# Optimization experiments

Hardware: AMD Instinct MI355X
Metric: run time of the kernel (lower is better)

The kernel has to match this reference:

```python
import jax, jax.numpy as jnp
import numpy as np

N_COMPANY, N_INDUSTRY, E = 20000, 500, 8192
CC, CI, D, H = 256, 128, 256, 4


def setup_inputs() -> dict:
    key = jax.random.key(0)
    ks = jax.random.split(key, 14)
    p = lambda k, shape: (jax.random.normal(k, shape, jnp.float32) * 0.02)
    company_x = jax.random.normal(ks[0], (N_COMPANY, CC), jnp.float32)
    industry_x = jax.random.normal(ks[1], (N_INDUSTRY, CI), jnp.float32)
    src = jax.random.randint(ks[2], (E,), 0, N_COMPANY)
    tgt = jax.random.randint(ks[3], (E,), 0, N_INDUSTRY)
    edge_index = jnp.stack([src, tgt]).astype(jnp.int64)
    return {
        "company_x": company_x,
        "industry_x": industry_x,
        "edge_index": edge_index,
        "Wc": p(ks[4], (D, CC)), "bc": jnp.zeros((D,), jnp.float32),
        "Wi": p(ks[5], (D, CI)), "bi": jnp.zeros((D,), jnp.float32),
        "w_in": p(ks[6], (3 * D, D)), "b_in": jnp.zeros((3 * D,), jnp.float32),
        "w_out": p(ks[7], (D, D)), "b_out": jnp.zeros((D,), jnp.float32),
        "gamma": jnp.ones((D,), jnp.float32), "beta": jnp.zeros((D,), jnp.float32),
    }


def reference(company_x, industry_x, edge_index, Wc, bc, Wi, bi, w_in, b_in, w_out, b_out, gamma, beta):
    company_h = company_x @ Wc.T + bc          # [N, D]
    industry_h = industry_x @ Wi.T + bi        # [M, D]
    src, tgt = edge_index[0], edge_index[1]
    e = src.shape[0]
    d = company_h.shape[-1]
    hd = d // H

    q_in = company_h[src]                      # [E, D] gather
    kv_in = industry_h[tgt]                    # [E, D] gather

    wq, wk, wv = jnp.split(w_in, 3, axis=0)
    bq, bk, bv = jnp.split(b_in, 3)
    qh = (q_in @ wq.T + bq).reshape(e, H, hd)
    kh = (kv_in @ wk.T + bk).reshape(e, H, hd)
    vh = (kv_in @ wv.T + bv).reshape(e, H, hd)

    scale = 1.0 / jnp.sqrt(jnp.float32(hd))
    scores = jnp.einsum("qhd,khd->hqk", qh * scale, kh)   # [H, E, E]
    attn = jax.nn.softmax(scores, axis=-1)
    ctx = jnp.einsum("hqk,khd->qhd", attn, vh).reshape(e, d)
    attn_out = ctx @ w_out.T + b_out                        # [E, D]

    agg = jax.ops.segment_sum(attn_out, src, num_segments=company_h.shape[0])
    counts = jax.ops.segment_sum(jnp.ones((e,), jnp.float32), src, num_segments=company_h.shape[0])
    pooled = agg / (counts[:, None] + 1e-6)

    out = company_h + pooled
    mean = out.mean(-1, keepdims=True)
    var = out.var(-1, keepdims=True)
    return (out - mean) / jnp.sqrt(var + 1e-5) * gamma + beta
```

## Files before the change

### kernel.cpp

```cpp
#include <hip/hip_runtime.h>

#define E_EDGES 8192
#define N_COMP  20000
#define N_IND   500
#define NKEYS   512

typedef short bf16x8 __attribute__((ext_vector_type(8)));
typedef float f32x4  __attribute__((ext_vector_type(4)));

static __device__ __forceinline__ unsigned short f2bf(float v) {
    unsigned u = __builtin_bit_cast(unsigned, v);
    u = (u + 0x7FFFu + ((u >> 16) & 1u)) >> 16;
    return (unsigned short)u;
}

static __device__ __forceinline__ void cvt8(const float* __restrict__ s,
                                            unsigned short* __restrict__ d) {
    float4 a = *(const float4*)s;
    float4 b = *(const float4*)(s + 4);
    bf16x8 o;
    o[0] = (short)f2bf(a.x); o[1] = (short)f2bf(a.y);
    o[2] = (short)f2bf(a.z); o[3] = (short)f2bf(a.w);
    o[4] = (short)f2bf(b.x); o[5] = (short)f2bf(b.y);
    o[6] = (short)f2bf(b.z); o[7] = (short)f2bf(b.w);
    *(bf16x8*)d = o;
}

static __device__ __forceinline__ bf16x8 cvt8r(const float* __restrict__ s) {
    float4 a = *(const float4*)s;
    float4 b = *(const float4*)(s + 4);
    bf16x8 v;
    v[0] = (short)f2bf(a.x); v[1] = (short)f2bf(a.y);
    v[2] = (short)f2bf(a.z); v[3] = (short)f2bf(a.w);
    v[4] = (short)f2bf(b.x); v[5] = (short)f2bf(b.y);
    v[6] = (short)f2bf(b.z); v[7] = (short)f2bf(b.w);
    return v;
}

#define SWZ(r)   (((r) & 7) << 4)
#define SWZ4(r)  ((((r) >> 1) & 3) << 4)

static __device__ __forceinline__ void stage_f32(const float* src, char* base,
                                                 int sr, int sc) {
    *(bf16x8*)(base + ((sr * 64 + sc * 2) ^ SWZ(sr))) = cvt8r(src);
}

__global__ __launch_bounds__(256) void prep(
    const int* __restrict__ src, const int* __restrict__ tgt,
    const float* __restrict__ Wc, const float* __restrict__ Wi,
    const float* __restrict__ w_out, const float* __restrict__ w_in,
    const float* __restrict__ bc, const float* __restrict__ bi,
    const float* __restrict__ b_in,
    float* __restrict__ csrc, float* __restrict__ ctgt,
    unsigned short* __restrict__ Wc_bf, unsigned short* __restrict__ wout_bf,
    unsigned short* __restrict__ WcT_bf, unsigned short* __restrict__ Wi_bf,
    unsigned short* __restrict__ wkv_bf, float* __restrict__ beff)
{
    const int bid = blockIdx.x, tid = threadIdx.x;
    if (bid < 32) {
        int e = bid * 256 + tid;
        atomicAdd(&csrc[src[e]], 1.0f);
        atomicAdd(&ctgt[tgt[e]], 1.0f);
    } else if (bid < 64) {
        long i = ((long)(bid - 32) * 256 + tid) * 8;
        cvt8(Wc + i, Wc_bf + i);
    } else if (bid < 96) {
        long i = ((long)(bid - 64) * 256 + tid) * 8;
        cvt8(w_out + i, wout_bf + i);
    } else if (bid < 128) {
        long o = ((long)(bid - 96) * 256 + tid) * 8;
        int c = (int)(o >> 8), d0 = (int)(o & 255);
        bf16x8 v;
#pragma unroll
        for (int j = 0; j < 8; j++) v[j] = (short)f2bf(Wc[(long)(d0 + j) * 256 + c]);
        *(bf16x8*)(WcT_bf + o) = v;
    } else if (bid < 144) {
        long i = ((long)(bid - 128) * 256 + tid) * 8;
        cvt8(Wi + i, Wi_bf + i);
    } else if (bid < 208) {
        long i = ((long)(bid - 144) * 256 + tid) * 8;
        cvt8(w_in + 65536 + i, wkv_bf + i);
    } else {
        int gi = (bid - 208) * 256 + tid;
        int e = gi >> 2, q = gi & 3;
        const float* base = (e < 256) ? bc : bi;
        const float* wr = w_in + (long)e * 256 + q * 64;
        const float* br = base + q * 64;
        float s = 0.f;
#pragma unroll
        for (int j = 0; j < 64; j += 4) {
            float4 w4 = *(const float4*)(wr + j);
            float4 b4 = *(const float4*)(br + j);
            s += w4.x * b4.x + w4.y * b4.y + w4.z * b4.z + w4.w * b4.w;
        }
        s += __shfl_xor(s, 1);
        s += __shfl_xor(s, 2);
        if (q == 0) beff[e] = s + b_in[e];
    }
}

__global__ __launch_bounds__(256) void fusedW(
    const float* __restrict__ w_in, const unsigned short* __restrict__ WcT_bf,
    const float* __restrict__ industry_x, const unsigned short* __restrict__ Wi_bf,
    const unsigned short* __restrict__ wkv_bf, const float* __restrict__ beff,
    const float* __restrict__ ctgt, const float* __restrict__ csrc,
    unsigned short* __restrict__ Wcq_bf, unsigned short* __restrict__ Kbuf,
    unsigned short* __restrict__ VTg,
    float* __restrict__ cntT, int* __restrict__ list, int* __restrict__ nlist)
{
    const int bid = blockIdx.x;
    if (bid >= 20) {
        int i = (bid - 20) * 256 + threadIdx.x;
        if (i < NKEYS) cntT[(i & 15) * 32 + (i >> 4)] = ctgt[i];
        if (i < N_COMP && csrc[i] > 0.f) {
            int k = atomicAdd(nlist, 1);
            list[k] = i;
        }
        return;
    }

    __shared__ char lds[48 * 1024];
    const int t = threadIdx.x, wv = t >> 6, lane = t & 63;
    const int g = lane >> 4, ln = lane & 15;
    const int sr = t >> 2, sc = (t & 3) * 8;

    if (bid < 4) {
        char* ab = lds;
        char* wb = lds + 4 * 1024;
        const int bm = bid * 64;
        f32x4 acc[16];
#pragma unroll
        for (int i = 0; i < 16; i++) acc[i] = (f32x4){0.f, 0.f, 0.f, 0.f};
        const float* aptr = w_in + (long)(bm + sr) * 256 + sc;
        for (int kc = 0; kc < 256; kc += 32) {
            __syncthreads();
            stage_f32(aptr + kc, ab, sr, sc);
#pragma unroll
            for (int p = 0; p < 4; p++) {
                int r = p * 64 + sr;
                *(bf16x8*)(wb + ((r * 64 + sc * 2) ^ SWZ(r))) =
                    *(const bf16x8*)(WcT_bf + (long)r * 256 + kc + sc);
            }
            __syncthreads();
            int ar = wv * 16 + ln;
            bf16x8 af = *(bf16x8*)(ab + ((ar * 64 + g * 16) ^ SWZ(ar)));
#pragma unroll
            for (int nj = 0; nj < 16; nj++) {
                int wr = nj * 16 + ln;
                bf16x8 bf = *(bf16x8*)(wb + ((wr * 64 + g * 16) ^ SWZ(wr)));
                acc[nj] = __builtin_amdgcn_mfma_f32_16x16x32_bf16(af, bf, acc[nj], 0, 0, 0);
            }
        }
#pragma unroll
        for (int nj = 0; nj < 16; nj++)
#pragma unroll
            for (int r = 0; r < 4; r++)
                Wcq_bf[(long)(bm + wv * 16 + g * 4 + r) * 256 + nj * 16 + ln] =
                    f2bf(acc[nj][r]);
        return;
    }

    const int rg = (bid - 4) >> 1, colh = (bid - 4) & 1;
    char* ab  = lds;
    char* wb1 = lds + 4 * 1024;
    char* ihb = lds + 16 * 1024;
    char* wb2 = lds;

    {
        f32x4 a1[16];
#pragma unroll
        for (int i = 0; i < 16; i++) a1[i] = (f32x4){0.f, 0.f, 0.f, 0.f};
        int arow = rg * 64 + sr; if (arow > N_IND - 1) arow = N_IND - 1;
        const float* aptr = industry_x + (long)arow * 128 + sc;
        for (int kc = 0; kc < 128; kc += 32) {
            __syncthreads();
            stage_f32(aptr + kc, ab, sr, sc);
#pragma unroll
            for (int p = 0; p < 4; p++) {
                int r = p * 64 + sr;
                *(bf16x8*)(wb1 + ((r * 64 + sc * 2) ^ SWZ(r))) =
                    *(const bf16x8*)(Wi_bf + (long)r * 128 + kc + sc);
            }
            __syncthreads();
            int ar = wv * 16 + ln;
            bf16x8 af = *(bf16x8*)(ab + ((ar * 64 + g * 16) ^ SWZ(ar)));
#pragma unroll
            for (int nj = 0; nj < 16; nj++) {
                int wr = nj * 16 + ln;
                bf16x8 bf = *(bf16x8*)(wb1 + ((wr * 64 + g * 16) ^ SWZ(wr)));
                a1[nj] = __builtin_amdgcn_mfma_f32_16x16x32_bf16(af, bf, a1[nj], 0, 0, 0);
            }
        }
        __syncthreads();
#pragma unroll
        for (int nj = 0; nj < 16; nj++)
#pragma unroll
            for (int r = 0; r < 4; r++) {
                int row = wv * 16 + g * 4 + r, col = nj * 16 + ln;
                *(unsigned short*)(ihb + ((row * 512 + col * 2) ^ SWZ(row))) =
                    f2bf(a1[nj][r]);
            }
    }
    __syncthreads();

    if (colh == 0) {
        f32x4 a2[16];
#pragma unroll
        for (int i = 0; i < 16; i++) a2[i] = (f32x4){0.f, 0.f, 0.f, 0.f};
        for (int kc = 0; kc < 256; kc += 32) {
            __syncthreads();
#pragma unroll
            for (int p = 0; p < 4; p++) {
                int r = p * 64 + sr;
                *(bf16x8*)(wb2 + ((r * 64 + sc * 2) ^ SWZ(r))) =
                    *(const bf16x8*)(wkv_bf + (long)r * 256 + kc + sc);
            }
            __syncthreads();
            int row = wv * 16 + ln;
            bf16x8 af = *(bf16x8*)(ihb + ((row * 512 + (kc + g * 8) * 2) ^ SWZ(row)));
#pragma unroll
            for (int nj = 0; nj < 16; nj++) {
                int wr = nj * 16 + ln;
                bf16x8 bf = *(bf16x8*)(wb2 + ((wr * 64 + g * 16) ^ SWZ(wr)));
                a2[nj] = __builtin_amdgcn_mfma_f32_16x16x32_bf16(af, bf, a2[nj], 0, 0, 0);
            }
        }
#pragma unroll
        for (int nj = 0; nj < 16; nj++)
#pragma unroll
            for (int r = 0; r < 4; r++) {
                int R = rg * 64 + wv * 16 + g * 4 + r, n = nj * 16 + ln;
                Kbuf[(long)R * 256 + n] = f2bf(a2[nj][r] + beff[256 + n]);
            }
    } else {
        const unsigned short* wp = wkv_bf + 65536;
        f32x4 a2[16];
#pragma unroll
        for (int i = 0; i < 16; i++) a2[i] = (f32x4){0.f, 0.f, 0.f, 0.f};
        for (int kc = 0; kc < 256; kc += 32) {
            __syncthreads();
#pragma unroll
            for (int p = 0; p < 4; p++) {
                int r = p * 64 + sr;
                *(bf16x8*)(wb2 + ((r * 64 + sc * 2) ^ SWZ(r))) =
                    *(const bf16x8*)(wp + (long)r * 256 + kc + sc);
            }
            __syncthreads();
#pragma unroll
            for (int mi = 0; mi < 4; mi++) {
                int arow = wv * 64 + mi * 16 + ln;
                bf16x8 af = *(bf16x8*)(wb2 + ((arow * 64 + g * 16) ^ SWZ(arow)));
#pragma unroll
                for (int t4 = 0; t4 < 4; t4++) {
                    int brow = t4 * 16 + ln;
                    bf16x8 bfr = *(bf16x8*)(ihb + ((brow * 512 + (kc + g * 8) * 2) ^ SWZ(brow)));
                    a2[mi * 4 + t4] = __builtin_amdgcn_mfma_f32_16x16x32_bf16(af, bfr, a2[mi * 4 + t4], 0, 0, 0);
                }
            }
        }
#pragma unroll
        for (int mi = 0; mi < 4; mi++)
#pragma unroll
            for (int t4 = 0; t4 < 4; t4++)
#pragma unroll
                for (int r = 0; r < 4; r++) {
                    int nrow = wv * 64 + mi * 16 + g * 4 + r;
                    VTg[(long)nrow * 512 + rg * 64 + t4 * 16 + ln] =
                        f2bf(a2[mi * 4 + t4][r] + beff[512 + nrow]);
                }
    }
}

__global__ __launch_bounds__(256, 2) void megattn(
    const float* __restrict__ company_x,
    const unsigned short* __restrict__ Wcq,
    const float* __restrict__ beff,
    const unsigned short* __restrict__ Kbuf,
    const unsigned short* __restrict__ VTg,
    const float* __restrict__ cntT,
    const unsigned short* __restrict__ wout,
    const float* __restrict__ b_out,
    const int* __restrict__ list, const int* __restrict__ nlist,
    float* __restrict__ pooled)
{
    const int M = *nlist;
    const int bm = blockIdx.x * 16;
    if (bm >= M) return;

    __shared__ char lds[24576];
    const int t = threadIdx.x, h = t >> 6, lane = t & 63;
    const int g = lane >> 4, ln = lane & 15;
    char* qbase = lds + h * 2048;
    char* xbase = lds + 8192;
    char* pbase = lds + 16384 + h * 2048;

    {
        int row = t >> 4, c0 = (t & 15) * 16;
        int mr = bm + row; if (mr > M - 1) mr = M - 1;
        const float* src = company_x + (long)list[mr] * 256 + c0;
        *(bf16x8*)(xbase + ((row * 512 + c0 * 2) ^ SWZ(row))) = cvt8r(src);
        *(bf16x8*)(xbase + ((row * 512 + c0 * 2 + 16) ^ SWZ(row))) = cvt8r(src + 8);
    }
    __syncthreads();

    bf16x8 qf0, qf1;
    {
        f32x4 qa[4];
#pragma unroll
        for (int i = 0; i < 4; i++) qa[i] = (f32x4){0.f, 0.f, 0.f, 0.f};
#pragma unroll
        for (int kc = 0; kc < 256; kc += 32) {
            bf16x8 af = *(bf16x8*)(xbase + ((ln * 512 + (kc + g * 8) * 2) ^ SWZ(ln)));
#pragma unroll
            for (int nj = 0; nj < 4; nj++) {
                bf16x8 bf = *(const bf16x8*)(Wcq + (long)(h * 64 + nj * 16 + ln) * 256 + kc + g * 8);
                qa[nj] = __builtin_amdgcn_mfma_f32_16x16x32_bf16(af, bf, qa[nj], 0, 0, 0);
            }
        }
#pragma unroll
        for (int nj = 0; nj < 4; nj++)
#pragma unroll
            for (int r = 0; r < 4; r++) {
                int row = g * 4 + r, col = nj * 16 + ln;
                *(unsigned short*)(qbase + ((row * 128 + col * 2) ^ SWZ(row))) =
                    f2bf((qa[nj][r] + beff[h * 64 + col]) * 0.125f);
            }
        qf0 = *(bf16x8*)(qbase + ((ln * 128 + g * 16) ^ SWZ(ln)));
        qf1 = *(bf16x8*)(qbase + ((ln * 128 + 64 + g * 16) ^ SWZ(ln)));
    }

    f32x4 acc[4];
#pragma unroll
    for (int i = 0; i < 4; i++) acc[i] = (f32x4){0.f, 0.f, 0.f, 0.f};
    float mreg[4] = {-1e30f, -1e30f, -1e30f, -1e30f};
    float lreg[4] = {0.f, 0.f, 0.f, 0.f};

#pragma unroll
    for (int tile = 0; tile < 2; tile++) {
        f32x4 S[8][2];
#pragma unroll
        for (int c = 0; c < 8; c++)
#pragma unroll
            for (int sub = 0; sub < 2; sub++) {
                const unsigned short* kr =
                    Kbuf + (long)(tile * 256 + c * 32 + sub * 16 + ln) * 256 + h * 64 + g * 8;
                bf16x8 k0 = *(const bf16x8*)(kr);
                bf16x8 k1 = *(const bf16x8*)(kr + 32);
                f32x4 s = (f32x4){0.f, 0.f, 0.f, 0.f};
                s = __builtin_amdgcn_mfma_f32_16x16x32_bf16(qf0, k0, s, 0, 0, 0);
                s = __builtin_amdgcn_mfma_f32_16x16x32_bf16(qf1, k1, s, 0, 0, 0);
                S[c][sub] = s;
            }

        float cnt[16];
        {
            const float* cp = cntT + ln * 32 + tile * 16;
#pragma unroll
            for (int j4 = 0; j4 < 4; j4++) {
                float4 c4 = *(const float4*)(cp + j4 * 4);
                cnt[j4 * 4 + 0] = c4.x; cnt[j4 * 4 + 1] = c4.y;
                cnt[j4 * 4 + 2] = c4.z; cnt[j4 * 4 + 3] = c4.w;
            }
        }

        float tm[4] = {-1e30f, -1e30f, -1e30f, -1e30f};
#pragma unroll
        for (int c = 0; c < 8; c++)
#pragma unroll
            for (int sub = 0; sub < 2; sub++)
#pragma unroll
                for (int r = 0; r < 4; r++) tm[r] = fmaxf(tm[r], S[c][sub][r]);
#pragma unroll
        for (int st = 1; st < 16; st <<= 1)
#pragma unroll
            for (int r = 0; r < 4; r++) tm[r] = fmaxf(tm[r], __shfl_xor(tm[r], st));

        float corr[4];
#pragma unroll
        for (int r = 0; r < 4; r++) {
            float mn = fmaxf(mreg[r], tm[r]);
            corr[r] = __expf(mreg[r] - mn);
            mreg[r] = mn;
        }

        float ps[4] = {0.f, 0.f, 0.f, 0.f};
#pragma unroll
        for (int c = 0; c < 8; c++)
#pragma unroll
            for (int sub = 0; sub < 2; sub++) {
                float cv = cnt[c * 2 + sub];
#pragma unroll
                for (int r = 0; r < 4; r++) {
                    float p = cv * __expf(S[c][sub][r] - mreg[r]);
                    S[c][sub][r] = p;
                    ps[r] += p;
                }
            }
#pragma unroll
        for (int st = 1; st < 16; st <<= 1)
#pragma unroll
            for (int r = 0; r < 4; r++) ps[r] += __shfl_xor(ps[r], st);
#pragma unroll
        for (int r = 0; r < 4; r++) lreg[r] = lreg[r] * corr[r] + ps[r];
#pragma unroll
        for (int i = 0; i < 4; i++)
#pragma unroll
            for (int r = 0; r < 4; r++) acc[i][r] *= corr[r];

#pragma unroll
        for (int c = 0; c < 8; c++) {
            char* pb = pbase + (c & 1) * 1024;
#pragma unroll
            for (int sub = 0; sub < 2; sub++)
#pragma unroll
                for (int r = 0; r < 4; r++) {
                    int row = g * 4 + r;
                    *(unsigned short*)(pb + ((row * 64 + (sub * 16 + ln) * 2) ^ SWZ4(row))) =
                        f2bf(S[c][sub][r]);
                }
            bf16x8 pa = *(bf16x8*)(pb + ((ln * 64 + g * 16) ^ SWZ4(ln)));
#pragma unroll
            for (int t4 = 0; t4 < 4; t4++) {
                bf16x8 vf = *(const bf16x8*)(
                    VTg + (long)(h * 64 + t4 * 16 + ln) * 512 + tile * 256 + c * 32 + g * 8);
                acc[t4] = __builtin_amdgcn_mfma_f32_16x16x32_bf16(pa, vf, acc[t4], 0, 0, 0);
            }
        }
    }

#pragma unroll
    for (int t4 = 0; t4 < 4; t4++)
#pragma unroll
        for (int r = 0; r < 4; r++) {
            int row = g * 4 + r, col = t4 * 16 + ln;
            *(unsigned short*)(qbase + ((row * 128 + col * 2) ^ SWZ(row))) =
                f2bf(acc[t4][r] / lreg[r]);
        }
    __syncthreads();

    {
        f32x4 oa[4];
#pragma unroll
        for (int i = 0; i < 4; i++) oa[i] = (f32x4){0.f, 0.f, 0.f, 0.f};
#pragma unroll
        for (int kc = 0; kc < 256; kc += 32) {
            int hs = kc >> 6;
            int off = (kc & 63) + g * 8;
            bf16x8 af = *(bf16x8*)(lds + hs * 2048 + ((ln * 128 + off * 2) ^ SWZ(ln)));
#pragma unroll
            for (int nj = 0; nj < 4; nj++) {
                bf16x8 bf = *(const bf16x8*)(wout + (long)(h * 64 + nj * 16 + ln) * 256 + kc + g * 8);
                oa[nj] = __builtin_amdgcn_mfma_f32_16x16x32_bf16(af, bf, oa[nj], 0, 0, 0);
            }
        }
#pragma unroll
        for (int nj = 0; nj < 4; nj++) {
            int n = h * 64 + nj * 16 + ln;
            float bv = b_out[n];
#pragma unroll
            for (int r = 0; r < 4; r++) {
                int R = bm + g * 4 + r;
                if (R < M)
                    pooled[(long)list[R] * 256 + n] = oa[nj][r] + bv;
            }
        }
    }
}

__global__ __launch_bounds__(256) void gemm_ln(
    const float* __restrict__ A, const unsigned short* __restrict__ W,
    const float* __restrict__ bias,
    const float* __restrict__ pooled, const float* __restrict__ csrc,
    const float* __restrict__ gamma, const float* __restrict__ beta,
    float* __restrict__ out, int M, int K)
{
    __shared__ unsigned short As[64 * 32];
    __shared__ unsigned short Ws[256 * 32];
    char* abase = (char*)As;
    char* wbase = (char*)Ws;

    const int bm = blockIdx.x * 64;
    const int t = threadIdx.x;
    const int wv = t >> 6, lane = t & 63, g = lane >> 4, ln = lane & 15;

    f32x4 acc[16];
#pragma unroll
    for (int i = 0; i < 16; i++) acc[i] = (f32x4){0.f, 0.f, 0.f, 0.f};

    const int sr = t >> 2;
    const int sc = (t & 3) * 8;
    int arow = bm + sr; if (arow > M - 1) arow = M - 1;
    const float* aptr = A + (long)arow * K + sc;

    for (int kc = 0; kc < K; kc += 32) {
        __syncthreads();
        stage_f32(aptr + kc, abase, sr, sc);
#pragma unroll
        for (int p = 0; p < 4; p++) {
            int r = p * 64 + sr;
            *(bf16x8*)(wbase + ((r * 64 + sc * 2) ^ SWZ(r))) =
                *(const bf16x8*)(W + (long)r * K + kc + sc);
        }
        __syncthreads();

        const int ar = wv * 16 + ln;
        bf16x8 af = *(bf16x8*)(abase + ((ar * 64 + g * 16) ^ SWZ(ar)));
#pragma unroll
        for (int nj = 0; nj < 16; nj++) {
            int wr = nj * 16 + ln;
            bf16x8 bf = *(bf16x8*)(wbase + ((wr * 64 + g * 16) ^ SWZ(wr)));
            acc[nj] = __builtin_amdgcn_mfma_f32_16x16x32_bf16(af, bf, acc[nj], 0, 0, 0);
        }
    }

#pragma unroll
    for (int r = 0; r < 4; r++) {
        int R = bm + wv * 16 + g * 4 + r;
        bool valid = R < M;
        int Rc = valid ? R : 0;
        float cntv = csrc[Rc];
        float factor = (valid && cntv > 0.f) ? cntv / (cntv + 1e-6f) : 0.f;

        float v[16];
        float sum = 0.f, sq = 0.f;
#pragma unroll
        for (int nj = 0; nj < 16; nj++) {
            int n = nj * 16 + ln;
            float x = acc[nj][r] + bias[n] + factor * pooled[(long)Rc * 256 + n];
            v[nj] = x;
            sum += x;
            sq  += x * x;
        }
#pragma unroll
        for (int st = 1; st < 16; st <<= 1) {
            sum += __shfl_xor(sum, st);
            sq  += __shfl_xor(sq,  st);
        }
        float mean = sum * (1.0f / 256.0f);
        float var  = sq * (1.0f / 256.0f) - mean * mean;
        float rstd = rsqrtf(var + 1e-5f);
        if (valid) {
#pragma unroll
            for (int nj = 0; nj < 16; nj++) {
                int n = nj * 16 + ln;
                out[(long)R * 256 + n] = (v[nj] - mean) * rstd * gamma[n] + beta[n];
            }
        }
    }
}

extern "C" void kernel_launch(void* const* d_in, const int* in_sizes, int n_in,
                              void* d_out, int out_size, void* d_ws, size_t ws_size,
                              hipStream_t stream)
{
    const float* company_x  = (const float*)d_in[0];
    const float* industry_x = (const float*)d_in[1];
    const int*   edge       = (const int*)d_in[2];
    const float* Wc         = (const float*)d_in[3];
    const float* bc         = (const float*)d_in[4];
    const float* Wi         = (const float*)d_in[5];
    const float* bi         = (const float*)d_in[6];
    const float* w_in       = (const float*)d_in[7];
    const float* b_in       = (const float*)d_in[8];
    const float* w_out      = (const float*)d_in[9];
    const float* b_out      = (const float*)d_in[10];
    const float* gamma      = (const float*)d_in[11];
    const float* beta       = (const float*)d_in[12];
    float* out = (float*)d_out;

    const int* src = edge;
    const int* tgt = edge + E_EDGES;

    float* wf = (float*)d_ws;
    size_t o = 0;
    unsigned short* Wc_bf   = (unsigned short*)(wf + o); o += 32768;
    unsigned short* wout_bf = (unsigned short*)(wf + o); o += 32768;
    unsigned short* WcT_bf  = (unsigned short*)(wf + o); o += 32768;
    unsigned short* Wi_bf   = (unsigned short*)(wf + o); o += 16384;
    unsigned short* wkv_bf  = (unsigned short*)(wf + o); o += 65536;
    unsigned short* Wcq_bf  = (unsigned short*)(wf + o); o += 32768;
    unsigned short* Kbuf    = (unsigned short*)(wf + o); o += 65536;
    unsigned short* VTg     = (unsigned short*)(wf + o); o += 65536;
    float* pooled           = wf + o; o += (size_t)N_COMP * 256;
    float* beff             = wf + o; o += 768;
    float* cntT             = wf + o; o += NKEYS;
    int*   list             = (int*)(wf + o); o += E_EDGES;
    float* csrc             = wf + o; o += N_COMP;
    float* ctgt             = wf + o; o += NKEYS;
    int*   nlist            = (int*)(wf + o); o += 4;

    dim3 blk(256);

    hipMemsetAsync(csrc, 0, (N_COMP + NKEYS + 4) * sizeof(float), stream);

    prep<<<dim3(220), blk, 0, stream>>>(
        src, tgt, Wc, Wi, w_out, w_in, bc, bi, b_in,
        csrc, ctgt, Wc_bf, wout_bf, WcT_bf, Wi_bf, wkv_bf, beff);

    fusedW<<<dim3(99), blk, 0, stream>>>(
        w_in, WcT_bf, industry_x, Wi_bf, wkv_bf, beff, ctgt, csrc,
        Wcq_bf, Kbuf, VTg, cntT, list, nlist);

    megattn<<<dim3(E_EDGES / 16), blk, 0, stream>>>(
        company_x, Wcq_bf, beff, Kbuf, VTg, cntT, wout_bf, b_out,
        list, nlist, pooled);

    gemm_ln<<<dim3((N_COMP + 63) / 64), blk, 0, stream>>>(
        company_x, Wc_bf, bc, pooled, csrc, gamma, beta, out, N_COMP, 256);
}
```

Measured before the change: 103.5 us.

## Split attention key range across two wave groups with split-K softmax merge

The megattn block grows from 256 to 512 threads. Each head now gets two waves, and each wave handles one half of the 512 keys instead of looping over both tiles. Partial max, sum and context accumulators from the second half go through LDS and are merged with log-sum-exp rescaling. The output projection is then split across all 8 waves. This doubles the waves per block to hide latency, at the cost of more LDS (56KB), an extra barrier and the merge step, which may limit occupancy.

```diff
diff --git a/kernel.cpp b/kernel.cpp
--- a/kernel.cpp
+++ b/kernel.cpp
@@ -271,7 +271,7 @@
     }
 }
 
-__global__ __launch_bounds__(256, 2) void megattn(
+__global__ __launch_bounds__(512, 4) void megattn(
     const float* __restrict__ company_x,
     const unsigned short* __restrict__ Wcq,
     const float* __restrict__ beff,
@@ -287,19 +287,24 @@
     const int bm = blockIdx.x * 16;
     if (bm >= M) return;
 
-    __shared__ char lds[24576];
-    const int t = threadIdx.x, h = t >> 6, lane = t & 63;
-    const int g = lane >> 4, ln = lane & 15;
+    __shared__ char lds[57344];
+    const int t = threadIdx.x;
+    const int w = t >> 6;
+    const int h = w & 3;
+    const int ks = w >> 2;
+    const int lane = t & 63, g = lane >> 4, ln = lane & 15;
+
     char* qbase = lds + h * 2048;
     char* xbase = lds + 8192;
-    char* pbase = lds + 16384 + h * 2048;
+    char* pbase = lds + 16384 + w * 2048;
+    float* macc = (float*)(lds + 32768) + h * 1024;
+    float* mml  = (float*)(lds + 49152) + h * 512;
 
     {
-        int row = t >> 4, c0 = (t & 15) * 16;
+        int row = t >> 5, c0 = (t & 31) * 8;
         int mr = bm + row; if (mr > M - 1) mr = M - 1;
         const float* src = company_x + (long)list[mr] * 256 + c0;
         *(bf16x8*)(xbase + ((row * 512 + c0 * 2) ^ SWZ(row))) = cvt8r(src);
-        *(bf16x8*)(xbase + ((row * 512 + c0 * 2 + 16) ^ SWZ(row))) = cvt8r(src + 8);
     }
     __syncthreads();
 
@@ -322,140 +327,149 @@
 #pragma unroll
             for (int r = 0; r < 4; r++) {
                 int row = g * 4 + r, col = nj * 16 + ln;
+                *(unsigned short*)(pbase + ((row * 128 + col * 2) ^ SWZ(row))) =
+                    f2bf((qa[nj][r] + beff[h * 64 + col]) * 0.125f);
+            }
+        qf0 = *(bf16x8*)(pbase + ((ln * 128 + g * 16) ^ SWZ(ln)));
+        qf1 = *(bf16x8*)(pbase + ((ln * 128 + 64 + g * 16) ^ SWZ(ln)));
+    }
+
+    f32x4 S[8][2];
+#pragma unroll
+    for (int c = 0; c < 8; c++)
+#pragma unroll
+        for (int sub = 0; sub < 2; sub++) {
+            const unsigned short* kr =
+                Kbuf + (long)(ks * 256 + c * 32 + sub * 16 + ln) * 256 + h * 64 + g * 8;
+            bf16x8 k0 = *(const bf16x8*)(kr);
+            bf16x8 k1 = *(const bf16x8*)(kr + 32);
+            f32x4 s = (f32x4){0.f, 0.f, 0.f, 0.f};
+            s = __builtin_amdgcn_mfma_f32_16x16x32_bf16(qf0, k0, s, 0, 0, 0);
+            s = __builtin_amdgcn_mfma_f32_16x16x32_bf16(qf1, k1, s, 0, 0, 0);
+            S[c][sub] = s;
+        }
+
+    float cnt[16];
+    {
+        const float* cp = cntT + ln * 32 + ks * 16;
+#pragma unroll
+        for (int j4 = 0; j4 < 4; j4++) {
+            float4 c4 = *(const float4*)(cp + j4 * 4);
+            cnt[j4 * 4 + 0] = c4.x; cnt[j4 * 4 + 1] = c4.y;
+            cnt[j4 * 4 + 2] = c4.z; cnt[j4 * 4 + 3] = c4.w;
+        }
+    }
+
+    float tm[4] = {-1e30f, -1e30f, -1e30f, -1e30f};
+#pragma unroll
+    for (int c = 0; c < 8; c++)
+#pragma unroll
+        for (int sub = 0; sub < 2; sub++)
+#pragma unroll
+            for (int r = 0; r < 4; r++) tm[r] = fmaxf(tm[r], S[c][sub][r]);
+#pragma unroll
+    for (int st = 1; st < 16; st <<= 1)
+#pragma unroll
+        for (int r = 0; r < 4; r++) tm[r] = fmaxf(tm[r], __shfl_xor(tm[r], st));
+
+    float ps[4] = {0.f, 0.f, 0.f, 0.f};
+#pragma unroll
+    for (int c = 0; c < 8; c++)
+#pragma unroll
+        for (int sub = 0; sub < 2; sub++) {
+            float cv = cnt[c * 2 + sub];
+#pragma unroll
+            for (int r = 0; r < 4; r++) {
+                float p = cv * __expf(S[c][sub][r] - tm[r]);
+                S[c][sub][r] = p;
+                ps[r] += p;
+            }
+        }
+#pragma unroll
+    for (int st = 1; st < 16; st <<= 1)
+#pragma unroll
+        for (int r = 0; r < 4; r++) ps[r] += __shfl_xor(ps[r], st);
+
+    f32x4 acc[4];
+#pragma unroll
+    for (int i = 0; i < 4; i++) acc[i] = (f32x4){0.f, 0.f, 0.f, 0.f};
+#pragma unroll
+    for (int c = 0; c < 8; c++) {
+        char* pb = pbase + (c & 1) * 1024;
+#pragma unroll
+        for (int sub = 0; sub < 2; sub++)
+#pragma unroll
+            for (int r = 0; r < 4; r++) {
+                int row = g * 4 + r;
+                *(unsigned short*)(pb + ((row * 64 + (sub * 16 + ln) * 2) ^ SWZ4(row))) =
+                    f2bf(S[c][sub][r]);
+            }
+        bf16x8 pa = *(bf16x8*)(pb + ((ln * 64 + g * 16) ^ SWZ4(ln)));
+#pragma unroll
+        for (int t4 = 0; t4 < 4; t4++) {
+            bf16x8 vf = *(const bf16x8*)(
+                VTg + (long)(h * 64 + t4 * 16 + ln) * 512 + ks * 256 + c * 32 + g * 8);
+            acc[t4] = __builtin_amdgcn_mfma_f32_16x16x32_bf16(pa, vf, acc[t4], 0, 0, 0);
+        }
+    }
+
+    if (ks == 1) {
+#pragma unroll
+        for (int t4 = 0; t4 < 4; t4++)
+#pragma unroll
+            for (int r = 0; r < 4; r++)
+                macc[(t4 * 4 + r) * 64 + lane] = acc[t4][r];
+#pragma unroll
+        for (int r = 0; r < 4; r++) {
+            mml[r * 64 + lane] = tm[r];
+            mml[(4 + r) * 64 + lane] = ps[r];
+        }
+    }
+    __syncthreads();
+    if (ks == 0) {
+        float sc0[4], sc1[4];
+#pragma unroll
+        for (int r = 0; r < 4; r++) {
+            float m1 = mml[r * 64 + lane];
+            float l1 = mml[(4 + r) * 64 + lane];
+            float mn = fmaxf(tm[r], m1);
+            float c0 = __expf(tm[r] - mn);
+            float c1 = __expf(m1 - mn);
+            float inv = 1.0f / (ps[r] * c0 + l1 * c1);
+            sc0[r] = c0 * inv;
+            sc1[r] = c1 * inv;
+        }
+#pragma unroll
+        for (int t4 = 0; t4 < 4; t4++)
+#pragma unroll
+            for (int r = 0; r < 4; r++) {
+                float ctxv = acc[t4][r] * sc0[r] + macc[(t4 * 4 + r) * 64 + lane] * sc1[r];
+                int row = g * 4 + r, col = t4 * 16 + ln;
                 *(unsigned short*)(qbase + ((row * 128 + col * 2) ^ SWZ(row))) =
-                    f2bf((qa[nj][r] + beff[h * 64 + col]) * 0.125f);
-            }
-        qf0 = *(bf16x8*)(qbase + ((ln * 128 + g * 16) ^ SWZ(ln)));
-        qf1 = *(bf16x8*)(qbase + ((ln * 128 + 64 + g * 16) ^ SWZ(ln)));
-    }
-
-    f32x4 acc[4];
-#pragma unroll
-    for (int i = 0; i < 4; i++) acc[i] = (f32x4){0.f, 0.f, 0.f, 0.f};
-    float mreg[4] = {-1e30f, -1e30f, -1e30f, -1e30f};
-    float lreg[4] = {0.f, 0.f, 0.f, 0.f};
-
-#pragma unroll
-    for (int tile = 0; tile < 2; tile++) {
-        f32x4 S[8][2];
-#pragma unroll
-        for (int c = 0; c < 8; c++)
-#pragma unroll
-            for (int sub = 0; sub < 2; sub++) {
-                const unsigned short* kr =
-                    Kbuf + (long)(tile * 256 + c * 32 + sub * 16 + ln) * 256 + h * 64 + g * 8;
-                bf16x8 k0 = *(const bf16x8*)(kr);
-                bf16x8 k1 = *(const bf16x8*)(kr + 32);
-                f32x4 s = (f32x4){0.f, 0.f, 0.f, 0.f};
-                s = __builtin_amdgcn_mfma_f32_16x16x32_bf16(qf0, k0, s, 0, 0, 0);
-                s = __builtin_amdgcn_mfma_f32_16x16x32_bf16(qf1, k1, s, 0, 0, 0);
-                S[c][sub] = s;
-            }
-
-        float cnt[16];
-        {
-            const float* cp = cntT + ln * 32 + tile * 16;
-#pragma unroll
-            for (int j4 = 0; j4 < 4; j4++) {
-                float4 c4 = *(const float4*)(cp + j4 * 4);
-                cnt[j4 * 4 + 0] = c4.x; cnt[j4 * 4 + 1] = c4.y;
-                cnt[j4 * 4 + 2] = c4.z; cnt[j4 * 4 + 3] = c4.w;
-            }
-        }
-
-        float tm[4] = {-1e30f, -1e30f, -1e30f, -1e30f};
-#pragma unroll
-        for (int c = 0; c < 8; c++)
-#pragma unroll
-            for (int sub = 0; sub < 2; sub++)
-#pragma unroll
-                for (int r = 0; r < 4; r++) tm[r] = fmaxf(tm[r], S[c][sub][r]);
-#pragma unroll
-        for (int st = 1; st < 16; st <<= 1)
-#pragma unroll
-            for (int r = 0; r < 4; r++) tm[r] = fmaxf(tm[r], __shfl_xor(tm[r], st));
-
-        float corr[4];
-#pragma unroll
-        for (int r = 0; r < 4; r++) {
-            float mn = fmaxf(mreg[r], tm[r]);
-            corr[r] = __expf(mreg[r] - mn);
-            mreg[r] = mn;
-        }
-
-        float ps[4] = {0.f, 0.f, 0.f, 0.f};
-#pragma unroll
-        for (int c = 0; c < 8; c++)
-#pragma unroll
-            for (int sub = 0; sub < 2; sub++) {
-                float cv = cnt[c * 2 + sub];
-#pragma unroll
-                for (int r = 0; r < 4; r++) {
-                    float p = cv * __expf(S[c][sub][r] - mreg[r]);
-                    S[c][sub][r] = p;
-                    ps[r] += p;
-                }
-            }
-#pragma unroll
-        for (int st = 1; st < 16; st <<= 1)
-#pragma unroll
-            for (int r = 0; r < 4; r++) ps[r] += __shfl_xor(ps[r], st);
-#pragma unroll
-        for (int r = 0; r < 4; r++) lreg[r] = lreg[r] * corr[r] + ps[r];
-#pragma unroll
-        for (int i = 0; i < 4; i++)
-#pragma unroll
-            for (int r = 0; r < 4; r++) acc[i][r] *= corr[r];
-
-#pragma unroll
-        for (int c = 0; c < 8; c++) {
-            char* pb = pbase + (c & 1) * 1024;
-#pragma unroll
-            for (int sub = 0; sub < 2; sub++)
-#pragma unroll
-                for (int r = 0; r < 4; r++) {
-                    int row = g * 4 + r;
-                    *(unsigned short*)(pb + ((row * 64 + (sub * 16 + ln) * 2) ^ SWZ4(row))) =
-                        f2bf(S[c][sub][r]);
-                }
-            bf16x8 pa = *(bf16x8*)(pb + ((ln * 64 + g * 16) ^ SWZ4(ln)));
-#pragma unroll
-            for (int t4 = 0; t4 < 4; t4++) {
-                bf16x8 vf = *(const bf16x8*)(
-                    VTg + (long)(h * 64 + t4 * 16 + ln) * 512 + tile * 256 + c * 32 + g * 8);
-                acc[t4] = __builtin_amdgcn_mfma_f32_16x16x32_bf16(pa, vf, acc[t4], 0, 0, 0);
-            }
-        }
-    }
-
-#pragma unroll
-    for (int t4 = 0; t4 < 4; t4++)
-#pragma unroll
-        for (int r = 0; r < 4; r++) {
-            int row = g * 4 + r, col = t4 * 16 + ln;
-            *(unsigned short*)(qbase + ((row * 128 + col * 2) ^ SWZ(row))) =
-                f2bf(acc[t4][r] / lreg[r]);
-        }
+                    f2bf(ctxv);
+            }
+    }
     __syncthreads();
 
     {
-        f32x4 oa[4];
-#pragma unroll
-        for (int i = 0; i < 4; i++) oa[i] = (f32x4){0.f, 0.f, 0.f, 0.f};
+        f32x4 oa[2];
+#pragma unroll
+        for (int i = 0; i < 2; i++) oa[i] = (f32x4){0.f, 0.f, 0.f, 0.f};
 #pragma unroll
         for (int kc = 0; kc < 256; kc += 32) {
             int hs = kc >> 6;
             int off = (kc & 63) + g * 8;
             bf16x8 af = *(bf16x8*)(lds + hs * 2048 + ((ln * 128 + off * 2) ^ SWZ(ln)));
 #pragma unroll
-            for (int nj = 0; nj < 4; nj++) {
-                bf16x8 bf = *(const bf16x8*)(wout + (long)(h * 64 + nj * 16 + ln) * 256 + kc + g * 8);
+            for (int nj = 0; nj < 2; nj++) {
+                int n = w * 32 + nj * 16 + ln;
+                bf16x8 bf = *(const bf16x8*)(wout + (long)n * 256 + kc + g * 8);
                 oa[nj] = __builtin_amdgcn_mfma_f32_16x16x32_bf16(af, bf, oa[nj], 0, 0, 0);
             }
         }
 #pragma unroll
-        for (int nj = 0; nj < 4; nj++) {
-            int n = h * 64 + nj * 16 + ln;
+        for (int nj = 0; nj < 2; nj++) {
+            int n = w * 32 + nj * 16 + ln;
             float bv = b_out[n];
 #pragma unroll
             for (int r = 0; r < 4; r++) {
@@ -589,22 +603,20 @@
     float* ctgt             = wf + o; o += NKEYS;
     int*   nlist            = (int*)(wf + o); o += 4;
 
-    dim3 blk(256);
-
     hipMemsetAsync(csrc, 0, (N_COMP + NKEYS + 4) * sizeof(float), stream);
 
-    prep<<<dim3(220), blk, 0, stream>>>(
+    prep<<<dim3(220), dim3(256), 0, stream>>>(
         src, tgt, Wc, Wi, w_out, w_in, bc, bi, b_in,
         csrc, ctgt, Wc_bf, wout_bf, WcT_bf, Wi_bf, wkv_bf, beff);
 
-    fusedW<<<dim3(99), blk, 0, stream>>>(
+    fusedW<<<dim3(99), dim3(256), 0, stream>>>(
         w_in, WcT_bf, industry_x, Wi_bf, wkv_bf, beff, ctgt, csrc,
         Wcq_bf, Kbuf, VTg, cntT, list, nlist);
 
-    megattn<<<dim3(E_EDGES / 16), blk, 0, stream>>>(
+    megattn<<<dim3(E_EDGES / 16), dim3(512), 0, stream>>>(
         company_x, Wcq_bf, beff, Kbuf, VTg, cntT, wout_bf, b_out,
         list, nlist, pooled);
 
-    gemm_ln<<<dim3((N_COMP + 63) / 64), blk, 0, stream>>>(
+    gemm_ln<<<dim3((N_COMP + 63) / 64), dim3(256), 0, stream>>>(
         company_x, Wc_bf, bc, pooled, csrc, gamma, beta, out, N_COMP, 256);
 }
```

Result: slower. 115.4 us (+11.5%).

## Split attention per head across blocks with LDS-staged K/V and separate out-projection

Applied to the files above, without the earlier changes.

The fused attention kernel is replaced by one block per (row-tile, head) that stages that head's full K and V^T (512 keys) into 144KB of dynamic LDS. The four waves each handle a quarter of the keys, and their partial softmax results are merged through LDS. The output projection moves to a separate kernel that reads a bf16 ctx buffer from global memory. This aims to cut redundant global K/V reads and raise parallelism. In exchange, every block reloads 128KB of K/V, occupancy drops to one block per CU, and there is an extra launch and a ctx round trip.

```diff
diff --git a/kernel.cpp b/kernel.cpp
--- a/kernel.cpp
+++ b/kernel.cpp
@@ -271,198 +271,237 @@
     }
 }
 
-__global__ __launch_bounds__(256, 2) void megattn(
+__global__ __launch_bounds__(256, 1) void attn2(
     const float* __restrict__ company_x,
     const unsigned short* __restrict__ Wcq,
     const float* __restrict__ beff,
     const unsigned short* __restrict__ Kbuf,
     const unsigned short* __restrict__ VTg,
     const float* __restrict__ cntT,
-    const unsigned short* __restrict__ wout,
-    const float* __restrict__ b_out,
+    const int* __restrict__ list, const int* __restrict__ nlist,
+    unsigned short* __restrict__ ctx)
+{
+    extern __shared__ char lds[];
+    const int M = *nlist;
+    const int bm = blockIdx.x * 16;
+    if (bm >= M) return;
+    const int h = blockIdx.y;
+    const int t = threadIdx.x, w = t >> 6, lane = t & 63;
+    const int g = lane >> 4, ln = lane & 15;
+
+    char* kldp = lds;
+    char* vldp = lds + 65536;
+    char* xb   = lds + 131072;
+    char* qb   = lds + 139264 + w * 2048;
+
+#pragma unroll
+    for (int i = 0; i < 16; i++) {
+        int idx = i * 256 + t;
+        int key = idx >> 3, seg = idx & 7;
+        *(bf16x8*)(kldp + ((key * 128 + seg * 16) ^ SWZ(key))) =
+            *(const bf16x8*)(Kbuf + (long)key * 256 + h * 64 + seg * 8);
+        int row = idx >> 6, sg = idx & 63;
+        *(bf16x8*)(vldp + ((row * 1024 + sg * 16) ^ SWZ(row))) =
+            *(const bf16x8*)(VTg + (long)(h * 64 + row) * 512 + sg * 8);
+    }
+    {
+        int row = t >> 4, c0 = (t & 15) * 16;
+        int mr = bm + row; if (mr > M - 1) mr = M - 1;
+        const float* src = company_x + (long)list[mr] * 256 + c0;
+        *(bf16x8*)(xb + ((row * 512 + c0 * 2) ^ SWZ(row))) = cvt8r(src);
+        *(bf16x8*)(xb + ((row * 512 + c0 * 2 + 16) ^ SWZ(row))) = cvt8r(src + 8);
+    }
+    __syncthreads();
+
+    bf16x8 qf0, qf1;
+    {
+        f32x4 qa[4];
+#pragma unroll
+        for (int i = 0; i < 4; i++) qa[i] = (f32x4){0.f, 0.f, 0.f, 0.f};
+#pragma unroll
+        for (int kc = 0; kc < 256; kc += 32) {
+            bf16x8 af = *(bf16x8*)(xb + ((ln * 512 + (kc + g * 8) * 2) ^ SWZ(ln)));
+#pragma unroll
+            for (int nj = 0; nj < 4; nj++) {
+                bf16x8 bf = *(const bf16x8*)(Wcq + (long)(h * 64 + nj * 16 + ln) * 256 + kc + g * 8);
+                qa[nj] = __builtin_amdgcn_mfma_f32_16x16x32_bf16(af, bf, qa[nj], 0, 0, 0);
+            }
+        }
+#pragma unroll
+        for (int nj = 0; nj < 4; nj++)
+#pragma unroll
+            for (int r = 0; r < 4; r++) {
+                int row = g * 4 + r, col = nj * 16 + ln;
+                *(unsigned short*)(qb + ((row * 128 + col * 2) ^ SWZ(row))) =
+                    f2bf((qa[nj][r] + beff[h * 64 + col]) * 0.125f);
+            }
+        qf0 = *(bf16x8*)(qb + ((ln * 128 + g * 16) ^ SWZ(ln)));
+        qf1 = *(bf16x8*)(qb + ((ln * 128 + 64 + g * 16) ^ SWZ(ln)));
+    }
+
+    f32x4 S[4][2];
+#pragma unroll
+    for (int c = 0; c < 4; c++)
+#pragma unroll
+        for (int sub = 0; sub < 2; sub++) {
+            int key = w * 128 + c * 32 + sub * 16 + ln;
+            int sw = SWZ(key);
+            bf16x8 k0 = *(bf16x8*)(kldp + ((key * 128 + g * 16) ^ sw));
+            bf16x8 k1 = *(bf16x8*)(kldp + ((key * 128 + 64 + g * 16) ^ sw));
+            f32x4 s = (f32x4){0.f, 0.f, 0.f, 0.f};
+            s = __builtin_amdgcn_mfma_f32_16x16x32_bf16(qf0, k0, s, 0, 0, 0);
+            s = __builtin_amdgcn_mfma_f32_16x16x32_bf16(qf1, k1, s, 0, 0, 0);
+            S[c][sub] = s;
+        }
+
+    float cnt[8];
+    {
+        const float* cp = cntT + ln * 32 + w * 8;
+        float4 c0 = *(const float4*)(cp);
+        float4 c1 = *(const float4*)(cp + 4);
+        cnt[0] = c0.x; cnt[1] = c0.y; cnt[2] = c0.z; cnt[3] = c0.w;
+        cnt[4] = c1.x; cnt[5] = c1.y; cnt[6] = c1.z; cnt[7] = c1.w;
+    }
+
+    float tm[4] = {-1e30f, -1e30f, -1e30f, -1e30f};
+#pragma unroll
+    for (int c = 0; c < 4; c++)
+#pragma unroll
+        for (int sub = 0; sub < 2; sub++)
+#pragma unroll
+            for (int r = 0; r < 4; r++) tm[r] = fmaxf(tm[r], S[c][sub][r]);
+#pragma unroll
+    for (int st = 1; st < 16; st <<= 1)
+#pragma unroll
+        for (int r = 0; r < 4; r++) tm[r] = fmaxf(tm[r], __shfl_xor(tm[r], st));
+
+    float ps[4] = {0.f, 0.f, 0.f, 0.f};
+#pragma unroll
+    for (int c = 0; c < 4; c++)
+#pragma unroll
+        for (int sub = 0; sub < 2; sub++) {
+            float cv = cnt[c * 2 + sub];
+#pragma unroll
+            for (int r = 0; r < 4; r++) {
+                float p = cv * __expf(S[c][sub][r] - tm[r]);
+                S[c][sub][r] = p;
+                ps[r] += p;
+            }
+        }
+#pragma unroll
+    for (int st = 1; st < 16; st <<= 1)
+#pragma unroll
+        for (int r = 0; r < 4; r++) ps[r] += __shfl_xor(ps[r], st);
+
+    f32x4 acc[4];
+#pragma unroll
+    for (int i = 0; i < 4; i++) acc[i] = (f32x4){0.f, 0.f, 0.f, 0.f};
+#pragma unroll
+    for (int c = 0; c < 4; c++) {
+        char* pb = qb + (c & 1) * 1024;
+#pragma unroll
+        for (int sub = 0; sub < 2; sub++)
+#pragma unroll
+            for (int r = 0; r < 4; r++) {
+                int row = g * 4 + r;
+                *(unsigned short*)(pb + ((row * 64 + (sub * 16 + ln) * 2) ^ SWZ4(row))) =
+                    f2bf(S[c][sub][r]);
+            }
+        bf16x8 pa = *(bf16x8*)(pb + ((ln * 64 + g * 16) ^ SWZ4(ln)));
+#pragma unroll
+        for (int t4 = 0; t4 < 4; t4++) {
+            int row = t4 * 16 + ln;
+            bf16x8 vf = *(bf16x8*)(vldp +
+                ((row * 1024 + (w * 128 + c * 32 + g * 8) * 2) ^ SWZ(row)));
+            acc[t4] = __builtin_amdgcn_mfma_f32_16x16x32_bf16(pa, vf, acc[t4], 0, 0, 0);
+        }
+    }
+
+    __syncthreads();
+    if (w != 0) {
+        float* macc = (float*)(lds + 131072) + (w - 1) * 1024;
+        float* ml   = (float*)(lds + 143360) + (w - 1) * 32;
+#pragma unroll
+        for (int t4 = 0; t4 < 4; t4++)
+#pragma unroll
+            for (int r = 0; r < 4; r++)
+                macc[(g * 4 + r) * 64 + t4 * 16 + ln] = acc[t4][r];
+        if (ln == 0) {
+#pragma unroll
+            for (int r = 0; r < 4; r++) {
+                ml[g * 4 + r]      = tm[r];
+                ml[16 + g * 4 + r] = ps[r];
+            }
+        }
+    }
+    __syncthreads();
+    if (w == 0) {
+#pragma unroll
+        for (int o = 0; o < 3; o++) {
+            float* macc = (float*)(lds + 131072) + o * 1024;
+            float* ml   = (float*)(lds + 143360) + o * 32;
+#pragma unroll
+            for (int r = 0; r < 4; r++) {
+                int row = g * 4 + r;
+                float m1 = ml[row], l1 = ml[16 + row];
+                float mn = fmaxf(tm[r], m1);
+                float c0 = __expf(tm[r] - mn);
+                float c1 = __expf(m1 - mn);
+#pragma unroll
+                for (int t4 = 0; t4 < 4; t4++)
+                    acc[t4][r] = acc[t4][r] * c0 +
+                                 macc[row * 64 + t4 * 16 + ln] * c1;
+                ps[r] = ps[r] * c0 + l1 * c1;
+                tm[r] = mn;
+            }
+        }
+#pragma unroll
+        for (int t4 = 0; t4 < 4; t4++)
+#pragma unroll
+            for (int r = 0; r < 4; r++) {
+                int R = bm + g * 4 + r;
+                if (R < M)
+                    ctx[(long)R * 256 + h * 64 + t4 * 16 + ln] =
+                        f2bf(acc[t4][r] / ps[r]);
+            }
+    }
+}
+
+__global__ __launch_bounds__(256) void out_proj(
+    const unsigned short* __restrict__ ctx,
+    const unsigned short* __restrict__ wout, const float* __restrict__ b_out,
     const int* __restrict__ list, const int* __restrict__ nlist,
     float* __restrict__ pooled)
 {
     const int M = *nlist;
     const int bm = blockIdx.x * 16;
     if (bm >= M) return;
-
-    __shared__ char lds[24576];
     const int t = threadIdx.x, h = t >> 6, lane = t & 63;
     const int g = lane >> 4, ln = lane & 15;
-    char* qbase = lds + h * 2048;
-    char* xbase = lds + 8192;
-    char* pbase = lds + 16384 + h * 2048;
-
-    {
-        int row = t >> 4, c0 = (t & 15) * 16;
-        int mr = bm + row; if (mr > M - 1) mr = M - 1;
-        const float* src = company_x + (long)list[mr] * 256 + c0;
-        *(bf16x8*)(xbase + ((row * 512 + c0 * 2) ^ SWZ(row))) = cvt8r(src);
-        *(bf16x8*)(xbase + ((row * 512 + c0 * 2 + 16) ^ SWZ(row))) = cvt8r(src + 8);
-    }
-    __syncthreads();
-
-    bf16x8 qf0, qf1;
-    {
-        f32x4 qa[4];
-#pragma unroll
-        for (int i = 0; i < 4; i++) qa[i] = (f32x4){0.f, 0.f, 0.f, 0.f};
-#pragma unroll
-        for (int kc = 0; kc < 256; kc += 32) {
-            bf16x8 af = *(bf16x8*)(xbase + ((ln * 512 + (kc + g * 8) * 2) ^ SWZ(ln)));
-#pragma unroll
-            for (int nj = 0; nj < 4; nj++) {
-                bf16x8 bf = *(const bf16x8*)(Wcq + (long)(h * 64 + nj * 16 + ln) * 256 + kc + g * 8);
-                qa[nj] = __builtin_amdgcn_mfma_f32_16x16x32_bf16(af, bf, qa[nj], 0, 0, 0);
-            }
-        }
-#pragma unroll
-        for (int nj = 0; nj < 4; nj++)
-#pragma unroll
-            for (int r = 0; r < 4; r++) {
-                int row = g * 4 + r, col = nj * 16 + ln;
-                *(unsigned short*)(qbase + ((row * 128 + col * 2) ^ SWZ(row))) =
-                    f2bf((qa[nj][r] + beff[h * 64 + col]) * 0.125f);
-            }
-        qf0 = *(bf16x8*)(qbase + ((ln * 128 + g * 16) ^ SWZ(ln)));
-        qf1 = *(bf16x8*)(qbase + ((ln * 128 + 64 + g * 16) ^ SWZ(ln)));
-    }
-
-    f32x4 acc[4];
-#pragma unroll
-    for (int i = 0; i < 4; i++) acc[i] = (f32x4){0.f, 0.f, 0.f, 0.f};
-    float mreg[4] = {-1e30f, -1e30f, -1e30f, -1e30f};
-    float lreg[4] = {0.f, 0.f, 0.f, 0.f};
-
-#pragma unroll
-    for (int tile = 0; tile < 2; tile++) {
-        f32x4 S[8][2];
-#pragma unroll
-        for (int c = 0; c < 8; c++)
-#pragma unroll
-            for (int sub = 0; sub < 2; sub++) {
-                const unsigned short* kr =
-                    Kbuf + (long)(tile * 256 + c * 32 + sub * 16 + ln) * 256 + h * 64 + g * 8;
-                bf16x8 k0 = *(const bf16x8*)(kr);
-                bf16x8 k1 = *(const bf16x8*)(kr + 32);
-                f32x4 s = (f32x4){0.f, 0.f, 0.f, 0.f};
-                s = __builtin_amdgcn_mfma_f32_16x16x32_bf16(qf0, k0, s, 0, 0, 0);
-                s = __builtin_amdgcn_mfma_f32_16x16x32_bf16(qf1, k1, s, 0, 0, 0);
-                S[c][sub] = s;
-            }
-
-        float cnt[16];
-        {
-            const float* cp = cntT + ln * 32 + tile * 16;
-#pragma unroll
-            for (int j4 = 0; j4 < 4; j4++) {
-                float4 c4 = *(const float4*)(cp + j4 * 4);
-                cnt[j4 * 4 + 0] = c4.x; cnt[j4 * 4 + 1] = c4.y;
-                cnt[j4 * 4 + 2] = c4.z; cnt[j4 * 4 + 3] = c4.w;
-            }
-        }
-
-        float tm[4] = {-1e30f, -1e30f, -1e30f, -1e30f};
-#pragma unroll
-        for (int c = 0; c < 8; c++)
-#pragma unroll
-            for (int sub = 0; sub < 2; sub++)
-#pragma unroll
-                for (int r = 0; r < 4; r++) tm[r] = fmaxf(tm[r], S[c][sub][r]);
-#pragma unroll
-        for (int st = 1; st < 16; st <<= 1)
-#pragma unroll
-            for (int r = 0; r < 4; r++) tm[r] = fmaxf(tm[r], __shfl_xor(tm[r], st));
-
-        float corr[4];
+
+    int arow = bm + ln; if (arow > M - 1) arow = M - 1;
+
+    f32x4 oa[4];
+#pragma unroll
+    for (int i = 0; i < 4; i++) oa[i] = (f32x4){0.f, 0.f, 0.f, 0.f};
+#pragma unroll
+    for (int kc = 0; kc < 256; kc += 32) {
+        bf16x8 af = *(const bf16x8*)(ctx + (long)arow * 256 + kc + g * 8);
+#pragma unroll
+        for (int nj = 0; nj < 4; nj++) {
+            bf16x8 bf = *(const bf16x8*)(wout + (long)(h * 64 + nj * 16 + ln) * 256 + kc + g * 8);
+            oa[nj] = __builtin_amdgcn_mfma_f32_16x16x32_bf16(af, bf, oa[nj], 0, 0, 0);
+        }
+    }
+#pragma unroll
+    for (int nj = 0; nj < 4; nj++) {
+        int n = h * 64 + nj * 16 + ln;
+        float bv = b_out[n];
 #pragma unroll
         for (int r = 0; r < 4; r++) {
-            float mn = fmaxf(mreg[r], tm[r]);
-            corr[r] = __expf(mreg[r] - mn);
-            mreg[r] = mn;
-        }
-
-        float ps[4] = {0.f, 0.f, 0.f, 0.f};
-#pragma unroll
-        for (int c = 0; c < 8; c++)
-#pragma unroll
-            for (int sub = 0; sub < 2; sub++) {
-                float cv = cnt[c * 2 + sub];
-#pragma unroll
-                for (int r = 0; r < 4; r++) {
-                    float p = cv * __expf(S[c][sub][r] - mreg[r]);
-                    S[c][sub][r] = p;
-                    ps[r] += p;
-                }
-            }
-#pragma unroll
-        for (int st = 1; st < 16; st <<= 1)
-#pragma unroll
-            for (int r = 0; r < 4; r++) ps[r] += __shfl_xor(ps[r], st);
-#pragma unroll
-        for (int r = 0; r < 4; r++) lreg[r] = lreg[r] * corr[r] + ps[r];
-#pragma unroll
-        for (int i = 0; i < 4; i++)
-#pragma unroll
-            for (int r = 0; r < 4; r++) acc[i][r] *= corr[r];
-
-#pragma unroll
-        for (int c = 0; c < 8; c++) {
-            char* pb = pbase + (c & 1) * 1024;
-#pragma unroll
-            for (int sub = 0; sub < 2; sub++)
-#pragma unroll
-                for (int r = 0; r < 4; r++) {
-                    int row = g * 4 + r;
-                    *(unsigned short*)(pb + ((row * 64 + (sub * 16 + ln) * 2) ^ SWZ4(row))) =
-                        f2bf(S[c][sub][r]);
-                }
-            bf16x8 pa = *(bf16x8*)(pb + ((ln * 64 + g * 16) ^ SWZ4(ln)));
-#pragma unroll
-            for (int t4 = 0; t4 < 4; t4++) {
-                bf16x8 vf = *(const bf16x8*)(
-                    VTg + (long)(h * 64 + t4 * 16 + ln) * 512 + tile * 256 + c * 32 + g * 8);
-                acc[t4] = __builtin_amdgcn_mfma_f32_16x16x32_bf16(pa, vf, acc[t4], 0, 0, 0);
-            }
-        }
-    }
-
-#pragma unroll
-    for (int t4 = 0; t4 < 4; t4++)
-#pragma unroll
-        for (int r = 0; r < 4; r++) {
-            int row = g * 4 + r, col = t4 * 16 + ln;
-            *(unsigned short*)(qbase + ((row * 128 + col * 2) ^ SWZ(row))) =
-                f2bf(acc[t4][r] / lreg[r]);
-        }
-    __syncthreads();
-
-    {
-        f32x4 oa[4];
-#pragma unroll
-        for (int i = 0; i < 4; i++) oa[i] = (f32x4){0.f, 0.f, 0.f, 0.f};
-#pragma unroll
-        for (int kc = 0; kc < 256; kc += 32) {
-            int hs = kc >> 6;
-            int off = (kc & 63) + g * 8;
-            bf16x8 af = *(bf16x8*)(lds + hs * 2048 + ((ln * 128 + off * 2) ^ SWZ(ln)));
-#pragma unroll
-            for (int nj = 0; nj < 4; nj++) {
-                bf16x8 bf = *(const bf16x8*)(wout + (long)(h * 64 + nj * 16 + ln) * 256 + kc + g * 8);
-                oa[nj] = __builtin_amdgcn_mfma_f32_16x16x32_bf16(af, bf, oa[nj], 0, 0, 0);
-            }
-        }
-#pragma unroll
-        for (int nj = 0; nj < 4; nj++) {
-            int n = h * 64 + nj * 16 + ln;
-            float bv = b_out[n];
-#pragma unroll
-            for (int r = 0; r < 4; r++) {
-                int R = bm + g * 4 + r;
-                if (R < M)
-                    pooled[(long)list[R] * 256 + n] = oa[nj][r] + bv;
-            }
+            int R = bm + g * 4 + r;
+            if (R < M)
+                pooled[(long)list[R] * 256 + n] = oa[nj][r] + bv;
         }
     }
 }
@@ -581,6 +620,7 @@
     unsigned short* Wcq_bf  = (unsigned short*)(wf + o); o += 32768;
     unsigned short* Kbuf    = (unsigned short*)(wf + o); o += 65536;
     unsigned short* VTg     = (unsigned short*)(wf + o); o += 65536;
+    unsigned short* ctx     = (unsigned short*)(wf + o); o += (size_t)E_EDGES * 128;
     float* pooled           = wf + o; o += (size_t)N_COMP * 256;
     float* beff             = wf + o; o += 768;
     float* cntT             = wf + o; o += NKEYS;
@@ -589,22 +629,22 @@
     float* ctgt             = wf + o; o += NKEYS;
     int*   nlist            = (int*)(wf + o); o += 4;
 
-    dim3 blk(256);
-
     hipMemsetAsync(csrc, 0, (N_COMP + NKEYS + 4) * sizeof(float), stream);
 
-    prep<<<dim3(220), blk, 0, stream>>>(
+    prep<<<dim3(220), dim3(256), 0, stream>>>(
         src, tgt, Wc, Wi, w_out, w_in, bc, bi, b_in,
         csrc, ctgt, Wc_bf, wout_bf, WcT_bf, Wi_bf, wkv_bf, beff);
 
-    fusedW<<<dim3(99), blk, 0, stream>>>(
+    fusedW<<<dim3(99), dim3(256), 0, stream>>>(
         w_in, WcT_bf, industry_x, Wi_bf, wkv_bf, beff, ctgt, csrc,
         Wcq_bf, Kbuf, VTg, cntT, list, nlist);
 
-    megattn<<<dim3(E_EDGES / 16), blk, 0, stream>>>(
-        company_x, Wcq_bf, beff, Kbuf, VTg, cntT, wout_bf, b_out,
-        list, nlist, pooled);
-
-    gemm_ln<<<dim3((N_COMP + 63) / 64), blk, 0, stream>>>(
+    attn2<<<dim3(512, 4), dim3(256), 147456, stream>>>(
+        company_x, Wcq_bf, beff, Kbuf, VTg, cntT, list, nlist, ctx);
+
+    out_proj<<<dim3(512), dim3(256), 0, stream>>>(
+        ctx, wout_bf, b_out, list, nlist, pooled);
+
+    gemm_ln<<<dim3((N_COMP + 63) / 64), dim3(256), 0, stream>>>(
         company_x, Wc_bf, bc, pooled, csrc, gamma, beta, out, N_COMP, 256);
 }
```

Measured after the change: 135.3 us. +30.8%, slower.
